# Kernel optimization log

Measured on AMD Instinct MI355X. Metric: run time of the kernel, lower is better.

Reference implementation:

```python
import jax, jax.numpy as jnp
import numpy as np

N_EMBD = 1024
N_HEAD = 16

def setup_inputs() -> dict:
    key = jax.random.key(0)
    k1, k2, k3, k4, k5 = jax.random.split(key, 5)
    C = N_EMBD
    s = 1.0 / np.sqrt(C)
    return {
        "x": jax.random.normal(k1, (2, 2048, C), dtype=jnp.float32),
        "W_attn": jax.random.normal(k2, (C, 3 * C), dtype=jnp.float32) * s,
        "b_attn": jax.random.normal(k3, (3 * C,), dtype=jnp.float32) * 0.02,
        "W_proj": jax.random.normal(k4, (C, C), dtype=jnp.float32) * s,
        "b_proj": jax.random.normal(k5, (C,), dtype=jnp.float32) * 0.02,
    }

def reference(x, W_attn, b_attn, W_proj, b_proj):
    B, T, C = x.shape
    nh = N_HEAD
    hs = C // nh
    qkv = x @ W_attn + b_attn                      # [B, T, 3C]
    q, k, v = jnp.split(qkv, 3, axis=-1)
    # [B, T, C] -> [B, nh, T, hs]
    def to_heads(t):
        return t.reshape(B, T, nh, hs).transpose(0, 2, 1, 3)
    q, k, v = to_heads(q), to_heads(k), to_heads(v)
    scale = 1.0 / np.sqrt(hs).astype(np.float32)
    att = jnp.einsum('bhqd,bhkd->bhqk', q, k) * scale   # [B, nh, T, T]
    causal = jnp.tril(jnp.ones((T, T), dtype=bool))
    att = jnp.where(causal, att, -jnp.inf)
    att = jax.nn.softmax(att, axis=-1)
    y = jnp.einsum('bhqk,bhkd->bhqd', att, v)           # [B, nh, T, hs]
    y = y.transpose(0, 2, 1, 3).reshape(B, T, C)
    return y @ W_proj + b_proj
```

## Files before the change

kernel.cpp:

```cpp
#include <hip/hip_runtime.h>
#include <hip/hip_bf16.h>
#include <math.h>

#define N_EMBD 1024
#define N_HEAD 16
#define HS 64
#define BT 4096
#define TSEQ 2048

typedef float f32x4 __attribute__((ext_vector_type(4)));
typedef short bf16x8 __attribute__((ext_vector_type(8)));
typedef unsigned short u16;

static __device__ __forceinline__ u16 f2bf(float f) {
  union { float f; unsigned int u; } c; c.f = f;
  unsigned int r = c.u + 0x7FFFu + ((c.u >> 16) & 1u);
  return (u16)(r >> 16);
}

static __device__ __forceinline__ u16 f2bf_fast(float f) {
  union { __hip_bfloat16 h; u16 u; } cv;
  cv.h = __float2bfloat16(f);
  return cv.u;
}

__global__ __launch_bounds__(256) void prep_all(
    const float* __restrict__ x, const float* __restrict__ Wa,
    const float* __restrict__ Wp, u16* __restrict__ xb,
    u16* __restrict__ Wat, u16* __restrict__ Wpt) {
  const int bid = blockIdx.x;
  const int t = threadIdx.x;
  if (bid < 4096) {
    int i = bid * 256 + t;
    float4 v = ((const float4*)x)[i];
    ushort4 o;
    o.x = f2bf(v.x); o.y = f2bf(v.y); o.z = f2bf(v.z); o.w = f2bf(v.w);
    ((ushort4*)xb)[i] = o;
    return;
  }
  __shared__ u16 Ls[32][36];
  const float* W; u16* Wt; int K, N, n0, k0;
  if (bid < 7168) {
    int g = bid - 4096;
    W = Wa; Wt = Wat; K = N_EMBD; N = 3 * N_EMBD;
    n0 = (g % 96) * 32; k0 = (g / 96) * 32;
  } else {
    int g = bid - 7168;
    W = Wp; Wt = Wpt; K = N_EMBD; N = N_EMBD;
    n0 = (g % 32) * 32; k0 = (g / 32) * 32;
  }
  {
    int kk = t >> 3, nn4 = (t & 7) * 4;
    float4 v = *(const float4*)(W + (size_t)(k0 + kk) * N + n0 + nn4);
    Ls[kk][nn4 + 0] = f2bf(v.x); Ls[kk][nn4 + 1] = f2bf(v.y);
    Ls[kk][nn4 + 2] = f2bf(v.z); Ls[kk][nn4 + 3] = f2bf(v.w);
  }
  __syncthreads();
  {
    int nn = t >> 3, kk4 = (t & 7) * 4;
    ushort4 o;
    o.x = Ls[kk4 + 0][nn]; o.y = Ls[kk4 + 1][nn];
    o.z = Ls[kk4 + 2][nn]; o.w = Ls[kk4 + 3][nn];
    *(ushort4*)(Wt + (size_t)(n0 + nn) * K + k0 + kk4) = o;
  }
}

#define BKS 32

__device__ __forceinline__ int swz(int row, int c) {
  return row * 4 + (c ^ ((row >> 1) & 3));
}

__device__ __forceinline__ void stage128x32(const u16* __restrict__ G, int ldk,
                                            u16* lds, int w, int lane) {
#pragma unroll
  for (int i = 0; i < 2; ++i) {
    int s = i * 256 + w * 64 + lane;
    int row = s >> 2, c = s & 3;
    int csrc = c ^ ((row >> 1) & 3);
    const u16* src = G + (size_t)row * ldk + csrc * 8;
    u16* dst = lds + (size_t)(i * 256 + w * 64) * 8;
    __builtin_amdgcn_global_load_lds(
        (const __attribute__((address_space(1))) void*)src,
        (__attribute__((address_space(3))) void*)dst, 16, 0, 0);
  }
}

#define GEMM_MAIN_LOOP(Aptr, Bptr, Kdim)                                        \
  __shared__ u16 sm[2][2][128 * BKS];                                           \
  const int tid = threadIdx.x, lane = tid & 63, w = tid >> 6;                   \
  const int wr = w >> 1, wc = w & 1, lrow = lane & 15, lhi = lane >> 4;         \
  const int _lin = blockIdx.y * gridDim.x + blockIdx.x;                         \
  const int _cpx = (gridDim.x * gridDim.y) >> 3;                                \
  const int _swz = (_lin & 7) * _cpx + (_lin >> 3);                             \
  const int bm = (_swz / gridDim.x) * 128, bn = (_swz % gridDim.x) * 128;       \
  f32x4 acc[4][4];                                                              \
  _Pragma("unroll") for (int i = 0; i < 4; ++i)                                 \
      _Pragma("unroll") for (int j = 0; j < 4; ++j)                             \
          acc[i][j] = (f32x4){0.f, 0.f, 0.f, 0.f};                              \
  stage128x32(Aptr + (size_t)bm * Kdim, Kdim, sm[0][0], w, lane);               \
  stage128x32(Bptr + (size_t)bn * Kdim, Kdim, sm[0][1], w, lane);               \
  __syncthreads();                                                              \
  const int NT = Kdim / BKS;                                                    \
  for (int t = 0; t < NT; ++t) {                                                \
    int cur = t & 1, nxt = cur ^ 1;                                             \
    if (t + 1 < NT) {                                                           \
      stage128x32(Aptr + (size_t)bm * Kdim + (t + 1) * BKS, Kdim, sm[nxt][0],   \
                  w, lane);                                                     \
      stage128x32(Bptr + (size_t)bn * Kdim + (t + 1) * BKS, Kdim, sm[nxt][1],   \
                  w, lane);                                                     \
    }                                                                           \
    const u16* As = sm[cur][0];                                                 \
    const u16* Bs = sm[cur][1];                                                 \
    bf16x8 af[4], bfr[4];                                                       \
    _Pragma("unroll") for (int mi = 0; mi < 4; ++mi) {                          \
      int row = wr * 64 + mi * 16 + lrow;                                       \
      af[mi] = *(const bf16x8*)(As + (size_t)swz(row, lhi) * 8);                \
    }                                                                           \
    _Pragma("unroll") for (int nj = 0; nj < 4; ++nj) {                          \
      int row = wc * 64 + nj * 16 + lrow;                                       \
      bfr[nj] = *(const bf16x8*)(Bs + (size_t)swz(row, lhi) * 8);               \
    }                                                                           \
    _Pragma("unroll") for (int mi = 0; mi < 4; ++mi)                            \
        _Pragma("unroll") for (int nj = 0; nj < 4; ++nj)                        \
            acc[mi][nj] = __builtin_amdgcn_mfma_f32_16x16x32_bf16(              \
                af[mi], bfr[nj], acc[mi][nj], 0, 0, 0);                         \
    __syncthreads();                                                            \
  }

__global__ __launch_bounds__(256) void gemm_qkv_bf16(
    const u16* __restrict__ Ab, const u16* __restrict__ Btr,
    const float* __restrict__ bias,
    u16* __restrict__ Qb, u16* __restrict__ Kb, u16* __restrict__ Vt) {
  GEMM_MAIN_LOOP(Ab, Btr, N_EMBD)
  const int sector = bn >> 10;
  const float QSC = 0.125f * 1.44269504f;
#pragma unroll
  for (int nj = 0; nj < 4; ++nj) {
    int n = bn + wc * 64 + nj * 16 + lrow;
    int h = (n & 1023) >> 6, d = n & 63;
    float bv = bias[n];
#pragma unroll
    for (int mi = 0; mi < 4; ++mi) {
      int mbase = bm + wr * 64 + mi * 16 + lhi * 4;
      int bb_ = mbase >> 11, tt = mbase & 2047;
      if (sector == 0) {
#pragma unroll
        for (int r = 0; r < 4; ++r)
          Qb[((size_t)(bb_ * 16 + h) * TSEQ + tt + r) * HS + d] =
              f2bf((acc[mi][nj][r] + bv) * QSC);
      } else if (sector == 1) {
#pragma unroll
        for (int r = 0; r < 4; ++r)
          Kb[((size_t)(bb_ * 16 + h) * TSEQ + tt + r) * HS + d] =
              f2bf(acc[mi][nj][r] + bv);
      } else {
        ushort4 o;
        o.x = f2bf(acc[mi][nj][0] + bv); o.y = f2bf(acc[mi][nj][1] + bv);
        o.z = f2bf(acc[mi][nj][2] + bv); o.w = f2bf(acc[mi][nj][3] + bv);
        *(ushort4*)(Vt + ((size_t)(bb_ * 16 + h) * HS + d) * TSEQ + tt) = o;
      }
    }
  }
}

__global__ __launch_bounds__(256) void gemm_proj_bf16(
    const u16* __restrict__ Ab, const u16* __restrict__ Btr,
    const float* __restrict__ bias, float* __restrict__ C) {
  GEMM_MAIN_LOOP(Ab, Btr, N_EMBD)
#pragma unroll
  for (int nj = 0; nj < 4; ++nj) {
    int n = bn + wc * 64 + nj * 16 + lrow;
    float bv = bias[n];
#pragma unroll
    for (int mi = 0; mi < 4; ++mi) {
      int mbase = bm + wr * 64 + mi * 16 + lhi * 4;
#pragma unroll
      for (int r = 0; r < 4; ++r)
        C[(size_t)(mbase + r) * N_EMBD + n] = acc[mi][nj][r] + bv;
    }
  }
}

__device__ __forceinline__ void stage_kv(const u16* __restrict__ Kh,
                                         const u16* __restrict__ Vh,
                                         int kb, u16* kbuf, u16* vbuf,
                                         int tid, int w) {
#pragma unroll
  for (int i = 0; i < 2; ++i) {
    int s = i * 256 + tid;
    int r = s >> 3, c = s & 7;
    int cs = c ^ (r & 7);
    const u16* ksrc = Kh + (size_t)(kb + r) * HS + cs * 8;
    u16* kdst = kbuf + (size_t)(i * 256 + (w << 6)) * 8;
    __builtin_amdgcn_global_load_lds(
        (const __attribute__((address_space(1))) void*)ksrc,
        (__attribute__((address_space(3))) void*)kdst, 16, 0, 0);
    const u16* vsrc = Vh + (size_t)r * TSEQ + kb + cs * 8;
    u16* vdst = vbuf + (size_t)(i * 256 + (w << 6)) * 8;
    __builtin_amdgcn_global_load_lds(
        (const __attribute__((address_space(1))) void*)vsrc,
        (__attribute__((address_space(3))) void*)vdst, 16, 0, 0);
  }
}

__global__ __launch_bounds__(256, 2) void attn_part(
    const u16* __restrict__ Qb, const u16* __restrict__ Kb,
    const u16* __restrict__ Vt, u16* __restrict__ Y,
    float* __restrict__ Pf, float* __restrict__ Lf) {
  __shared__ u16 Ks[2][64 * HS];
  __shared__ u16 Vs[2][64 * HS];
  __shared__ u16 Plds[4][32][72];

  const int tid  = threadIdx.x;
  const int lane = tid & 63;
  const int w    = tid >> 6;
  const int lrow = lane & 15;
  const int lhi  = lane >> 4;

  const int wg  = blockIdx.x;
  const int xcd = wg & 7;
  const int lin = wg >> 3;
  const int bhl = lin / 24;
  const int p   = lin % 24;
  int j, half, split;
  if (p < 16) { j = 15 - (p >> 1); half = p & 1; split = 1; }
  else        { j = 23 - p;        half = 0;     split = 0; }
  const int bh = (xcd << 2) | bhl;
  const int b  = bh >> 4, h = bh & 15;

  const u16* Qh = Qb + (size_t)bh * TSEQ * HS;
  const u16* Kh = Kb + (size_t)bh * TSEQ * HS;
  const u16* Vh = Vt + (size_t)bh * HS * TSEQ;

  const int q0 = j * 128 + w * 32;
  const int nsteps = split ? (j + 1) : (2 * j + 2);
  int kb = split ? (half * (j + 1) * 64) : 0;

  bf16x8 aq[4];
  aq[0] = *(const bf16x8*)(Qh + (size_t)(q0 + lrow) * HS + lhi * 8);
  aq[1] = *(const bf16x8*)(Qh + (size_t)(q0 + lrow) * HS + 32 + lhi * 8);
  aq[2] = *(const bf16x8*)(Qh + (size_t)(q0 + 16 + lrow) * HS + lhi * 8);
  aq[3] = *(const bf16x8*)(Qh + (size_t)(q0 + 16 + lrow) * HS + 32 + lhi * 8);

  bf16x8 ones;
#pragma unroll
  for (int i = 0; i < 8; ++i) ones[i] = (short)0x3F80;

  f32x4 o[2][4], ol[2];
#pragma unroll
  for (int sub = 0; sub < 2; ++sub) {
    ol[sub] = (f32x4){0.f, 0.f, 0.f, 0.f};
#pragma unroll
    for (int ds = 0; ds < 4; ++ds) o[sub][ds] = (f32x4){0.f, 0.f, 0.f, 0.f};
  }

  stage_kv(Kh, Vh, kb, Ks[0], Vs[0], tid, w);

  for (int t = 0; t < nsteps; ++t) {
    const int cur = t & 1;
    __syncthreads();
    if (t + 1 < nsteps)
      stage_kv(Kh, Vh, kb + 64, Ks[cur ^ 1], Vs[cur ^ 1], tid, w);

    const u16* Kc = Ks[cur];
    const u16* Vc = Vs[cur];

    f32x4 sacc[2][4];
#pragma unroll
    for (int s = 0; s < 4; ++s) {
      int r = s * 16 + lrow;
      bf16x8 k0 = *(const bf16x8*)(Kc + r * HS + ((lhi    ) ^ (r & 7)) * 8);
      bf16x8 k1 = *(const bf16x8*)(Kc + r * HS + ((lhi + 4) ^ (r & 7)) * 8);
      f32x4 z0 = (f32x4){0.f, 0.f, 0.f, 0.f};
      f32x4 z1 = (f32x4){0.f, 0.f, 0.f, 0.f};
      z0 = __builtin_amdgcn_mfma_f32_16x16x32_bf16(aq[0], k0, z0, 0, 0, 0);
      z0 = __builtin_amdgcn_mfma_f32_16x16x32_bf16(aq[1], k1, z0, 0, 0, 0);
      z1 = __builtin_amdgcn_mfma_f32_16x16x32_bf16(aq[2], k0, z1, 0, 0, 0);
      z1 = __builtin_amdgcn_mfma_f32_16x16x32_bf16(aq[3], k1, z1, 0, 0, 0);
      sacc[0][s] = z0; sacc[1][s] = z1;
    }

#pragma unroll
    for (int sub = 0; sub < 2; ++sub) {
      const int qbase = q0 + sub * 16;
      if (kb + 63 > qbase) {
#pragma unroll
        for (int s = 0; s < 4; ++s) {
          int kg = kb + 16 * s + lrow;
#pragma unroll
          for (int r = 0; r < 4; ++r)
            if (kg > qbase + lhi * 4 + r) sacc[sub][s][r] = -3.0e38f;
        }
      }
#pragma unroll
      for (int s = 0; s < 4; ++s)
#pragma unroll
        for (int r = 0; r < 4; ++r)
          Plds[w][sub * 16 + lhi * 4 + r][s * 16 + lrow] =
              f2bf_fast(exp2f(sacc[sub][s][r] - 16.0f));
    }

#pragma unroll
    for (int ks = 0; ks < 2; ++ks) {
      bf16x8 pa0 = *(const bf16x8*)&Plds[w][lrow][ks * 32 + lhi * 8];
      bf16x8 pa1 = *(const bf16x8*)&Plds[w][16 + lrow][ks * 32 + lhi * 8];
      ol[0] = __builtin_amdgcn_mfma_f32_16x16x32_bf16(pa0, ones, ol[0], 0, 0, 0);
      ol[1] = __builtin_amdgcn_mfma_f32_16x16x32_bf16(pa1, ones, ol[1], 0, 0, 0);
#pragma unroll
      for (int ds = 0; ds < 4; ++ds) {
        int vr = ds * 16 + lrow;
        bf16x8 vf = *(const bf16x8*)(Vc + vr * 64 + ((ks * 4 + lhi) ^ (vr & 7)) * 8);
        o[0][ds] = __builtin_amdgcn_mfma_f32_16x16x32_bf16(pa0, vf, o[0][ds], 0, 0, 0);
        o[1][ds] = __builtin_amdgcn_mfma_f32_16x16x32_bf16(pa1, vf, o[1][ds], 0, 0, 0);
      }
    }
    kb += 64;
  }

  if (!split) {
#pragma unroll
    for (int sub = 0; sub < 2; ++sub)
#pragma unroll
      for (int r = 0; r < 4; ++r) {
        float inv = 1.0f / ol[sub][r];
        int q = q0 + sub * 16 + lhi * 4 + r;
#pragma unroll
        for (int ds = 0; ds < 4; ++ds)
          Y[((size_t)(b * TSEQ + q)) * N_EMBD + h * HS + ds * 16 + lrow] =
              f2bf(o[sub][ds][r] * inv);
      }
  } else {
    const int slot = (((bh << 3) | (j - 8)) << 1) | half;
    float* orow = Pf + (size_t)slot * (128 * 64);
#pragma unroll
    for (int sub = 0; sub < 2; ++sub)
#pragma unroll
      for (int r = 0; r < 4; ++r) {
        int row = w * 32 + sub * 16 + lhi * 4 + r;
#pragma unroll
        for (int ds = 0; ds < 4; ++ds)
          orow[row * 64 + ds * 16 + lrow] = o[sub][ds][r];
        if (lrow == 0) Lf[slot * 128 + row] = ol[sub][r];
      }
  }
}

__global__ __launch_bounds__(256) void attn_combine(
    const float* __restrict__ Pf, const float* __restrict__ Lf,
    u16* __restrict__ Y) {
  const int bi = blockIdx.x;
  const int bh = bi >> 3, jj = 8 + (bi & 7);
  const int b  = bh >> 4, h = bh & 15;
  const int s0 = (((bh << 3) | (jj - 8)) << 1);
  const int tid = threadIdx.x;
  const int d   = tid & 63;
  const int rg  = tid >> 6;

  const float* o0 = Pf + (size_t)s0 * (128 * 64);
  const float* o1 = o0 + (128 * 64);
  for (int rr = 0; rr < 32; ++rr) {
    int row = rg * 32 + rr;
    float l = Lf[s0 * 128 + row] + Lf[(s0 + 1) * 128 + row];
    float o = o0[row * 64 + d] + o1[row * 64 + d];
    int q = jj * 128 + row;
    Y[((size_t)(b * TSEQ + q)) * N_EMBD + h * HS + d] = f2bf(o / l);
  }
}

extern "C" void kernel_launch(void* const* d_in, const int* in_sizes, int n_in,
                              void* d_out, int out_size, void* d_ws, size_t ws_size,
                              hipStream_t stream) {
  const float* x      = (const float*)d_in[0];
  const float* W_attn = (const float*)d_in[1];
  const float* b_attn = (const float*)d_in[2];
  const float* W_proj = (const float*)d_in[3];
  const float* b_proj = (const float*)d_in[4];
  float* out = (float*)d_out;

  u16* xb  = (u16*)d_ws;
  u16* Wat = xb  + (size_t)BT * N_EMBD;
  u16* Wpt = Wat + (size_t)3 * N_EMBD * N_EMBD;
  u16* Qb  = Wpt + (size_t)N_EMBD * N_EMBD;
  u16* Kb  = Qb  + (size_t)BT * N_EMBD;
  u16* Vt  = Kb  + (size_t)BT * N_EMBD;
  u16* yb  = Vt  + (size_t)BT * N_EMBD;
  float* Pf = (float*)(yb + (size_t)BT * N_EMBD);
  float* Lf = Pf + (size_t)512 * 128 * 64;

  prep_all<<<8192, 256, 0, stream>>>(x, W_attn, W_proj, xb, Wat, Wpt);
  {
    dim3 grid(3 * N_EMBD / 128, BT / 128);
    gemm_qkv_bf16<<<grid, 256, 0, stream>>>(xb, Wat, b_attn, Qb, Kb, Vt);
  }
  {
    attn_part<<<768, 256, 0, stream>>>(Qb, Kb, Vt, yb, Pf, Lf);
    attn_combine<<<256, 256, 0, stream>>>(Pf, Lf, yb);
  }
  {
    dim3 grid(N_EMBD / 128, BT / 128);
    gemm_proj_bf16<<<grid, 256, 0, stream>>>(yb, Wpt, b_proj, out);
  }
}
```

Measured before the change: 128.7 us.

## Rebalance split-KV attention with three-way and two-way query-tile splits

Changes the causal attention work split. The longest query tiles (j 10–15) now have their KV range cut into three parts, mid tiles (j 4–9) into two, and the shortest tiles run unsplit. This gives 1088 more evenly sized blocks instead of 768, which is meant to shorten the longest block and reduce tail imbalance. The combine kernel now sums up to three partials per row over 384 blocks. To hold the extra partial buffers, the dead xb/W_attn staging region of the workspace is reused. The cost is more partial-result traffic and more combine work.

```diff
diff --git a/kernel.cpp b/kernel.cpp
--- a/kernel.cpp
+++ b/kernel.cpp
@@ -207,7 +207,7 @@
 __global__ __launch_bounds__(256, 2) void attn_part(
     const u16* __restrict__ Qb, const u16* __restrict__ Kb,
     const u16* __restrict__ Vt, u16* __restrict__ Y,
-    float* __restrict__ Pf, float* __restrict__ Lf) {
+    float* PfLow, float* PfHi, float* __restrict__ Lf) {
   __shared__ u16 Ks[2][64 * HS];
   __shared__ u16 Vs[2][64 * HS];
   __shared__ u16 Plds[4][32][72];
@@ -221,21 +221,26 @@
   const int wg  = blockIdx.x;
   const int xcd = wg & 7;
   const int lin = wg >> 3;
-  const int bhl = lin / 24;
-  const int p   = lin % 24;
-  int j, half, split;
-  if (p < 16) { j = 15 - (p >> 1); half = p & 1; split = 1; }
-  else        { j = 23 - p;        half = 0;     split = 0; }
-  const int bh = (xcd << 2) | bhl;
-  const int b  = bh >> 4, h = bh & 15;
+  const int bhl = lin / 34;
+  const int id  = lin % 34;
+  const int bh  = (xcd << 2) | bhl;
+  const int b   = bh >> 4, h = bh & 15;
+
+  int j, part, cnt;
+  if (id < 18)      { j = 15 - id / 3;        part = id % 3;        cnt = 3; }
+  else if (id < 30) { j = 9 - (id - 18) / 2;  part = (id - 18) & 1; cnt = 2; }
+  else              { j = 33 - id;            part = 0;             cnt = 1; }
+  const int split  = (cnt > 1);
+  const int tsteps = 2 * j + 2;
+  const int s0 = (part * tsteps) / cnt;
+  const int s1 = ((part + 1) * tsteps) / cnt;
+  const int nsteps = s1 - s0;
 
   const u16* Qh = Qb + (size_t)bh * TSEQ * HS;
   const u16* Kh = Kb + (size_t)bh * TSEQ * HS;
   const u16* Vh = Vt + (size_t)bh * HS * TSEQ;
 
   const int q0 = j * 128 + w * 32;
-  const int nsteps = split ? (j + 1) : (2 * j + 2);
-  int kb = split ? (half * (j + 1) * 64) : 0;
 
   bf16x8 aq[4];
   aq[0] = *(const bf16x8*)(Qh + (size_t)(q0 + lrow) * HS + lhi * 8);
@@ -255,6 +260,7 @@
     for (int ds = 0; ds < 4; ++ds) o[sub][ds] = (f32x4){0.f, 0.f, 0.f, 0.f};
   }
 
+  int kb = s0 * 64;
   stage_kv(Kh, Vh, kb, Ks[0], Vs[0], tid, w);
 
   for (int t = 0; t < nsteps; ++t) {
@@ -331,8 +337,10 @@
               f2bf(o[sub][ds][r] * inv);
       }
   } else {
-    const int slot = (((bh << 3) | (j - 8)) << 1) | half;
-    float* orow = Pf + (size_t)slot * (128 * 64);
+    const int slot = bh * 30 + id;
+    float* orow = (slot < 448)
+                      ? (PfLow + (size_t)slot * 8192)
+                      : (PfHi + (size_t)(slot - 448) * 8192);
 #pragma unroll
     for (int sub = 0; sub < 2; ++sub)
 #pragma unroll
@@ -347,22 +355,31 @@
 }
 
 __global__ __launch_bounds__(256) void attn_combine(
-    const float* __restrict__ Pf, const float* __restrict__ Lf,
+    const float* PfLow, const float* PfHi, const float* __restrict__ Lf,
     u16* __restrict__ Y) {
   const int bi = blockIdx.x;
-  const int bh = bi >> 3, jj = 8 + (bi & 7);
+  const int bh = bi / 12, jj = 4 + (bi % 12);
   const int b  = bh >> 4, h = bh & 15;
-  const int s0 = (((bh << 3) | (jj - 8)) << 1);
+  int cnt, baseid;
+  if (jj >= 10) { cnt = 3; baseid = (15 - jj) * 3; }
+  else          { cnt = 2; baseid = 18 + (9 - jj) * 2; }
+  const int slot0 = bh * 30 + baseid;
+
   const int tid = threadIdx.x;
   const int d   = tid & 63;
   const int rg  = tid >> 6;
 
-  const float* o0 = Pf + (size_t)s0 * (128 * 64);
-  const float* o1 = o0 + (128 * 64);
   for (int rr = 0; rr < 32; ++rr) {
     int row = rg * 32 + rr;
-    float l = Lf[s0 * 128 + row] + Lf[(s0 + 1) * 128 + row];
-    float o = o0[row * 64 + d] + o1[row * 64 + d];
+    float l = 0.f, o = 0.f;
+    for (int k = 0; k < cnt; ++k) {
+      int slot = slot0 + k;
+      const float* orow = (slot < 448)
+                              ? (PfLow + (size_t)slot * 8192)
+                              : (PfHi + (size_t)(slot - 448) * 8192);
+      l += Lf[slot * 128 + row];
+      o += orow[row * 64 + d];
+    }
     int q = jj * 128 + row;
     Y[((size_t)(b * TSEQ + q)) * N_EMBD + h * HS + d] = f2bf(o / l);
   }
@@ -385,8 +402,9 @@
   u16* Kb  = Qb  + (size_t)BT * N_EMBD;
   u16* Vt  = Kb  + (size_t)BT * N_EMBD;
   u16* yb  = Vt  + (size_t)BT * N_EMBD;
-  float* Pf = (float*)(yb + (size_t)BT * N_EMBD);
-  float* Lf = Pf + (size_t)512 * 128 * 64;
+  float* PfLow = (float*)d_ws;
+  float* PfHi  = (float*)(yb + (size_t)BT * N_EMBD);
+  float* Lf    = PfHi + (size_t)512 * 8192;
 
   prep_all<<<8192, 256, 0, stream>>>(x, W_attn, W_proj, xb, Wat, Wpt);
   {
@@ -394,8 +412,8 @@
     gemm_qkv_bf16<<<grid, 256, 0, stream>>>(xb, Wat, b_attn, Qb, Kb, Vt);
   }
   {
-    attn_part<<<768, 256, 0, stream>>>(Qb, Kb, Vt, yb, Pf, Lf);
-    attn_combine<<<256, 256, 0, stream>>>(Pf, Lf, yb);
+    attn_part<<<1088, 256, 0, stream>>>(Qb, Kb, Vt, yb, PfLow, PfHi, Lf);
+    attn_combine<<<384, 256, 0, stream>>>(PfLow, PfHi, Lf, yb);
   }
   {
     dim3 grid(N_EMBD / 128, BT / 128);
```

After: 152.4 us. +18.4%, slower.
